# Kernel tuning notes

Measured on AMD Instinct MI355X. Metric: run time of the kernel, lower is better.

The kernel has to match this reference:

```python
import jax, jax.numpy as jnp
import numpy as np

# delta_rule mode: order=1, gate_type='k', linear=True, trick='derivative' (n=1 expansion is identity)
B, H, S, D = 1, 16, 4096, 64
CHUNK = 64  # max_chunk_size, divides S
EPS = 1e-6


def setup_inputs() -> dict:
    key = jax.random.key(0)
    kq, kk, kv, kb = jax.random.split(key, 4)
    return {
        "q": jax.random.normal(kq, (B, H, S, D), jnp.float32),
        "k": jax.random.normal(kk, (B, H, S, D), jnp.float32),
        "v": jax.random.normal(kv, (B, H, S, D), jnp.float32),
        "beta": jax.random.uniform(kb, (B, H, S), jnp.float32),
    }


def _ensure_stability(x, lo=-10000.0, hi=10000.0):
    c = (hi + lo) / 2
    x = jnp.clip(x, lo, hi)
    return jnp.nan_to_num(x, nan=c, posinf=hi, neginf=lo)


def _l2norm(x):
    return x / (jnp.linalg.norm(x, axis=-1, keepdims=True) + EPS)


def _forward(q, k, v, beta):
    Bq, Hq, Sq, Dq = q.shape
    C = CHUNK
    Nc = Sq // C
    q = _l2norm(q)
    k = _l2norm(k)
    # gate_type 'k': clamp(beta, 1e-6, 1-1e-6)
    g = jnp.clip(beta, EPS, 1.0 - EPS)[..., None]
    k_beta = k * g
    v_beta = v * g
    ch = lambda x: x.reshape(Bq, Hq, Nc, C, Dq)  # chunk_sequence
    qc, kc, kbc, vbc = map(ch, (q, k, k_beta, v_beta))

    # UT transform: attn = -(k_beta k^T) strictly lower; T = (I - attn)^{-1}
    # fast_invert_matrix (forward substitution) == unit-lower triangular solve
    attn = -jnp.einsum('bhnid,bhnjd->bhnij', kbc, kc)
    strict = jnp.tril(jnp.ones((C, C), bool), k=-1)
    attn = jnp.where(strict, attn, 0.0)
    eye = jnp.eye(C, dtype=q.dtype)
    Tm = jax.lax.linalg.triangular_solve(
        eye - attn, jnp.broadcast_to(eye, attn.shape),
        left_side=True, lower=True, unit_diagonal=True)
    W = jnp.einsum('bhnij,bhnjd->bhnid', Tm, kbc)
    U = jnp.einsum('bhnij,bhnjd->bhnid', Tm, vbc)

    # sequential_delta_product_scan, n_orders=1: per-token state == broadcast h0
    def step(h0, xs):
        q_c, w_c, u_c = xs  # each [B,H,C,D]; h0 [B,H,D,D]
        kth = jnp.einsum('bhcd,bhde->bhce', w_c, h0)      # w_s @ h_old per token
        u_val = u_c - kth
        o_inter = jnp.einsum('bhcd,bhde->bhce', q_c, h0)  # q_s @ h_old
        o_intra = q_c * u_val                              # elementwise, as in source
        # per-token Householder state update; only last token's state propagates (n_orders=1)
        h_new = h0 + w_c[:, :, -1, :, None] * u_val[:, :, -1, None, :]
        h_new = _ensure_stability(h_new)
        return h_new, o_intra + o_inter

    xs = (jnp.moveaxis(qc, 2, 0), jnp.moveaxis(W, 2, 0), jnp.moveaxis(U, 2, 0))
    h0 = jnp.zeros((Bq, Hq, Dq, Dq), q.dtype)
    _, outs = jax.lax.scan(step, h0, xs)  # [Nc, B, H, C, D]
    return jnp.moveaxis(outs, 0, 2).reshape(Bq, Hq, Sq, Dq)


def reference(q, k, v, beta):
    return _forward(q, k, v, beta)
```

## Files before the change

kernel.cpp:

```cpp
#include <hip/hip_runtime.h>
#include <math.h>

#define BHn 16
#define SLEN 4096
#define Dd 64
#define Cc 64
#define NCC 64
#define EPSF 1e-6f
#define PD 65

__global__ __launch_bounds__(256, 4) void kA(
    const float* __restrict__ kg, const float* __restrict__ vg,
    const float* __restrict__ betag, float* __restrict__ WTg, float* __restrict__ UTg,
    float* __restrict__ wlast, float* __restrict__ ulast)
{
    const int n = blockIdx.x, bh = blockIdx.y, tid = threadIdx.x;
    __shared__ float KT[64 * PD];
    __shared__ float SM[64 * PD];
    __shared__ float gl[64];

    const size_t base = ((size_t)bh * SLEN + (size_t)n * Cc) * Dd;

    if (tid < 64) {
        const float b = betag[(size_t)bh * SLEN + n * Cc + tid];
        gl[tid] = fminf(fmaxf(b, EPSF), 1.0f - EPSF);
    }
#pragma unroll
    for (int p = 0; p < 4; p++) {
        const int flat = p * 1024 + tid * 4;
        const int row = flat >> 6, d0 = flat & 63;
        const float4 a = *(const float4*)(kg + base + flat);
        float ss = a.x * a.x + a.y * a.y + a.z * a.z + a.w * a.w;
        ss += __shfl_xor(ss, 1); ss += __shfl_xor(ss, 2);
        ss += __shfl_xor(ss, 4); ss += __shfl_xor(ss, 8);
        const float inv = 1.0f / (sqrtf(ss) + EPSF);
        KT[(d0 + 0) * PD + row] = a.x * inv;
        KT[(d0 + 1) * PD + row] = a.y * inv;
        KT[(d0 + 2) * PD + row] = a.z * inv;
        KT[(d0 + 3) * PD + row] = a.w * inv;
    }
    __syncthreads();

    float sol[64];
    if (tid < 64) {
#pragma unroll
        for (int j4 = 0; j4 < 16; j4++) {
            const float4 t4 = *(const float4*)&KT[tid * PD + j4 * 4];
            sol[j4 * 4 + 0] = t4.x * gl[j4 * 4 + 0];
            sol[j4 * 4 + 1] = t4.y * gl[j4 * 4 + 1];
            sol[j4 * 4 + 2] = t4.z * gl[j4 * 4 + 2];
            sol[j4 * 4 + 3] = t4.w * gl[j4 * 4 + 3];
        }
    } else if (tid < 200) {
        const int t = tid - 64;
        int ti = (int)((sqrtf(8.0f * (float)t + 1.0f) - 1.0f) * 0.5f);
        while (ti * (ti + 1) / 2 > t) --ti;
        while ((ti + 1) * (ti + 2) / 2 <= t) ++ti;
        const int tj = t - ti * (ti + 1) / 2;
        const int i0 = ti * 4, j0 = tj * 4;
        float sa[4][4];
#pragma unroll
        for (int r = 0; r < 4; r++)
#pragma unroll
            for (int c2 = 0; c2 < 4; c2++) sa[r][c2] = 0.f;
        for (int d = 0; d < 64; d++) {
            const float4 a = *(const float4*)&KT[d * PD + i0];
            const float4 b = *(const float4*)&KT[d * PD + j0];
            const float av[4] = {a.x, a.y, a.z, a.w};
            const float bv[4] = {b.x, b.y, b.z, b.w};
#pragma unroll
            for (int r = 0; r < 4; r++)
#pragma unroll
                for (int c2 = 0; c2 < 4; c2++) sa[r][c2] += av[r] * bv[c2];
        }
#pragma unroll
        for (int r = 0; r < 4; r++) {
            const float gg = gl[i0 + r];
            *(float4*)&SM[(i0 + r) * PD + j0] =
                make_float4(sa[r][0] * gg, sa[r][1] * gg, sa[r][2] * gg, sa[r][3] * gg);
        }
    }
    __syncthreads();

#pragma unroll
    for (int p = 0; p < 4; p++) {
        const int flat = p * 1024 + tid * 4;
        const int row = flat >> 6, d0 = flat & 63;
        const float4 a = *(const float4*)(vg + base + flat);
        const float gg = gl[row];
        KT[(d0 + 0) * PD + row] = a.x * gg;
        KT[(d0 + 1) * PD + row] = a.y * gg;
        KT[(d0 + 2) * PD + row] = a.z * gg;
        KT[(d0 + 3) * PD + row] = a.w * gg;
    }
    __syncthreads();

    if (tid >= 64 && tid < 128) {
        const int c = tid - 64;
#pragma unroll
        for (int j4 = 0; j4 < 16; j4++) {
            const float4 t4 = *(const float4*)&KT[c * PD + j4 * 4];
            sol[j4 * 4 + 0] = t4.x; sol[j4 * 4 + 1] = t4.y;
            sol[j4 * 4 + 2] = t4.z; sol[j4 * 4 + 3] = t4.w;
        }
    }
    if (tid < 128) {
        const int c = tid & 63;
#pragma unroll
        for (int b = 0; b < 8; b++) {
            const int i0 = b * 8;
            float acc[8];
#pragma unroll
            for (int r = 0; r < 8; r++) acc[r] = sol[i0 + r];
#pragma unroll
            for (int j4 = 0; j4 < 2 * b; j4++) {
                const int j = j4 * 4;
                const float s0 = sol[j + 0], s1 = sol[j + 1];
                const float s2 = sol[j + 2], s3 = sol[j + 3];
#pragma unroll
                for (int r = 0; r < 8; r++) {
                    const float4 m4 = *(const float4*)&SM[(i0 + r) * PD + j];
                    acc[r] -= m4.x * s0 + m4.y * s1 + m4.z * s2 + m4.w * s3;
                }
            }
#pragma unroll
            for (int il = 1; il < 8; il++)
#pragma unroll
                for (int jl = 0; jl < il; jl++)
                    acc[il] -= SM[(i0 + il) * PD + i0 + jl] * acc[jl];
#pragma unroll
            for (int r = 0; r < 8; r++) sol[i0 + r] = acc[r];
        }
        float* dst = (tid < 64 ? WTg : UTg) +
                     (size_t)(bh * NCC + n) * Cc * Dd + (size_t)c * 64;
#pragma unroll
        for (int j4 = 0; j4 < 16; j4++)
            *(float4*)(dst + j4 * 4) = make_float4(sol[j4 * 4 + 0], sol[j4 * 4 + 1],
                                                   sol[j4 * 4 + 2], sol[j4 * 4 + 3]);
        float* lst = (tid < 64 ? wlast : ulast);
        lst[(size_t)(bh * NCC + n) * 64 + c] = sol[63];
    }
}

__global__ __launch_bounds__(256) void kB(
    const float* __restrict__ wlast, const float* __restrict__ ulast,
    float* __restrict__ Uvg)
{
    const int bh = blockIdx.x, tid = threadIdx.x;
    __shared__ float WL[64 * PD];
    __shared__ float UL[64 * PD];
    __shared__ float SM[64 * PD];
    const size_t gbase = (size_t)bh * NCC * 64;

#pragma unroll
    for (int p = 0; p < 4; p++) {
        const int flat = p * 1024 + tid * 4;
        const int m = flat >> 6, d = flat & 63;
        *(float4*)&WL[m * PD + d] = *(const float4*)(wlast + gbase + flat);
        *(float4*)&UL[m * PD + d] = *(const float4*)(ulast + gbase + flat);
    }
    __syncthreads();

    if (tid < 136) {
        int ti = (int)((sqrtf(8.0f * (float)tid + 1.0f) - 1.0f) * 0.5f);
        while (ti * (ti + 1) / 2 > tid) --ti;
        while ((ti + 1) * (ti + 2) / 2 <= tid) ++ti;
        const int tj = tid - ti * (ti + 1) / 2;
        const int i0 = ti * 4, j0 = tj * 4;
        float sa[4][4];
#pragma unroll
        for (int r = 0; r < 4; r++)
#pragma unroll
            for (int c2 = 0; c2 < 4; c2++) sa[r][c2] = 0.f;
        for (int d4 = 0; d4 < 16; d4++) {
            const int d = d4 * 4;
            float4 ar[4], bc[4];
#pragma unroll
            for (int r = 0; r < 4; r++) ar[r] = *(const float4*)&WL[(i0 + r) * PD + d];
#pragma unroll
            for (int c2 = 0; c2 < 4; c2++) bc[c2] = *(const float4*)&WL[(j0 + c2) * PD + d];
#pragma unroll
            for (int r = 0; r < 4; r++)
#pragma unroll
                for (int c2 = 0; c2 < 4; c2++)
                    sa[r][c2] += ar[r].x * bc[c2].x + ar[r].y * bc[c2].y +
                                 ar[r].z * bc[c2].z + ar[r].w * bc[c2].w;
        }
#pragma unroll
        for (int r = 0; r < 4; r++)
            *(float4*)&SM[(i0 + r) * PD + j0] =
                make_float4(sa[r][0], sa[r][1], sa[r][2], sa[r][3]);
    }
    __syncthreads();

    if (tid < 64) {
        const int e = tid;
        float sol[64];
#pragma unroll
        for (int m = 0; m < 64; m++) sol[m] = UL[m * PD + e];
#pragma unroll
        for (int b = 0; b < 8; b++) {
            const int i0 = b * 8;
            float acc[8];
#pragma unroll
            for (int r = 0; r < 8; r++) acc[r] = sol[i0 + r];
#pragma unroll
            for (int j4 = 0; j4 < 2 * b; j4++) {
                const int j = j4 * 4;
                const float s0 = sol[j + 0], s1 = sol[j + 1];
                const float s2 = sol[j + 2], s3 = sol[j + 3];
#pragma unroll
                for (int r = 0; r < 8; r++) {
                    const float4 m4 = *(const float4*)&SM[(i0 + r) * PD + j];
                    acc[r] -= m4.x * s0 + m4.y * s1 + m4.z * s2 + m4.w * s3;
                }
            }
#pragma unroll
            for (int il = 1; il < 8; il++)
#pragma unroll
                for (int jl = 0; jl < il; jl++)
                    acc[il] -= SM[(i0 + il) * PD + i0 + jl] * acc[jl];
#pragma unroll
            for (int r = 0; r < 8; r++) sol[i0 + r] = acc[r];
        }
#pragma unroll
        for (int m = 0; m < 64; m++) Uvg[gbase + (size_t)m * 64 + e] = sol[m];
    }
}

__global__ __launch_bounds__(256, 3) void kC(
    const float* __restrict__ qg, const float* __restrict__ WTg,
    const float* __restrict__ UTg, const float* __restrict__ wlast,
    const float* __restrict__ Uvg, float* __restrict__ outg)
{
    const int bx = blockIdx.x, bh = blockIdx.y, tid = threadIdx.x;
    __shared__ float X1[64 * 64];
    __shared__ float X2[64 * PD];
    __shared__ float HB[64 * 64];
    const size_t lbase = (size_t)bh * NCC * 64;
    const int t0 = (tid >> 4) * 4, e0 = (tid & 15) * 4;

    const int n = 63 - bx;
    const size_t qbase = ((size_t)bh * SLEN + (size_t)n * Cc) * Dd;
    const size_t wbase = (size_t)(bh * NCC + n) * Cc * Dd;

    float4 qa[4], wt[4];
    float qinv[4];
#pragma unroll
    for (int p = 0; p < 4; p++) {
        const int flat = p * 1024 + tid * 4;
        const int m = flat >> 6, d = flat & 63;
        *(float4*)&X1[m * 64 + d] = *(const float4*)(wlast + lbase + flat);
        *(float4*)&X2[m * PD + d] = *(const float4*)(Uvg + lbase + flat);
        qa[p] = *(const float4*)(qg + qbase + flat);
        float ss = qa[p].x * qa[p].x + qa[p].y * qa[p].y +
                   qa[p].z * qa[p].z + qa[p].w * qa[p].w;
        ss += __shfl_xor(ss, 1); ss += __shfl_xor(ss, 2);
        ss += __shfl_xor(ss, 4); ss += __shfl_xor(ss, 8);
        qinv[p] = 1.0f / (sqrtf(ss) + EPSF);
        wt[p] = *(const float4*)(WTg + wbase + flat);
    }
    __syncthreads();

    float ha[4][4];
#pragma unroll
    for (int r = 0; r < 4; r++)
#pragma unroll
        for (int c2 = 0; c2 < 4; c2++) ha[r][c2] = 0.f;
    for (int m = 0; m < n; m++) {
        const float4 a = *(const float4*)&X1[m * 64 + t0];
        const float4 b = *(const float4*)&X2[m * PD + e0];
        const float av[4] = {a.x, a.y, a.z, a.w};
        const float bv[4] = {b.x, b.y, b.z, b.w};
#pragma unroll
        for (int r = 0; r < 4; r++)
#pragma unroll
            for (int c2 = 0; c2 < 4; c2++) ha[r][c2] += av[r] * bv[c2];
    }
#pragma unroll
    for (int r = 0; r < 4; r++)
        *(float4*)&HB[(t0 + r) * 64 + e0] =
            make_float4(ha[r][0], ha[r][1], ha[r][2], ha[r][3]);
    __syncthreads();

#pragma unroll
    for (int p = 0; p < 4; p++) {
        const int flat = p * 1024 + tid * 4;
        const int d = flat >> 6, t = flat & 63;
        *(float4*)&X1[d * 64 + t] = wt[p];
        const int row = d, d0 = t;
        X2[(d0 + 0) * PD + row] = qa[p].x * qinv[p];
        X2[(d0 + 1) * PD + row] = qa[p].y * qinv[p];
        X2[(d0 + 2) * PD + row] = qa[p].z * qinv[p];
        X2[(d0 + 3) * PD + row] = qa[p].w * qinv[p];
    }
    __syncthreads();

    float kth[4][4], oin[4][4];
#pragma unroll
    for (int r = 0; r < 4; r++)
#pragma unroll
        for (int c2 = 0; c2 < 4; c2++) { kth[r][c2] = 0.f; oin[r][c2] = 0.f; }
#pragma unroll 4
    for (int d = 0; d < 64; d++) {
        const float4 wv = *(const float4*)&X1[d * 64 + t0];
        const float4 qv = *(const float4*)&X2[d * PD + t0];
        const float4 hv = *(const float4*)&HB[d * 64 + e0];
        const float wa[4] = {wv.x, wv.y, wv.z, wv.w};
        const float qa2[4] = {qv.x, qv.y, qv.z, qv.w};
        const float hv4[4] = {hv.x, hv.y, hv.z, hv.w};
#pragma unroll
        for (int r = 0; r < 4; r++)
#pragma unroll
            for (int c2 = 0; c2 < 4; c2++) {
                kth[r][c2] += wa[r] * hv4[c2];
                oin[r][c2] += qa2[r] * hv4[c2];
            }
    }

    float* oc = outg + qbase;
    float o4[4][4];
#pragma unroll
    for (int s = 0; s < 4; s++) {
        const float4 u4 = *(const float4*)(UTg + wbase + (size_t)(e0 + s) * 64 + t0);
        const float4 q4 = *(const float4*)&X2[(e0 + s) * PD + t0];
        o4[0][s] = q4.x * (u4.x - kth[0][s]) + oin[0][s];
        o4[1][s] = q4.y * (u4.y - kth[1][s]) + oin[1][s];
        o4[2][s] = q4.z * (u4.z - kth[2][s]) + oin[2][s];
        o4[3][s] = q4.w * (u4.w - kth[3][s]) + oin[3][s];
    }
#pragma unroll
    for (int r = 0; r < 4; r++)
        *(float4*)(oc + (size_t)(t0 + r) * 64 + e0) =
            make_float4(o4[r][0], o4[r][1], o4[r][2], o4[r][3]);
}

extern "C" void kernel_launch(void* const* d_in, const int* in_sizes, int n_in,
                              void* d_out, int out_size, void* d_ws, size_t ws_size,
                              hipStream_t stream) {
    const float* q    = (const float*)d_in[0];
    const float* k    = (const float*)d_in[1];
    const float* v    = (const float*)d_in[2];
    const float* beta = (const float*)d_in[3];
    float* out = (float*)d_out;

    float* WTg   = (float*)d_ws;
    float* UTg   = WTg + (size_t)BHn * NCC * Cc * Dd;
    float* wlast = UTg + (size_t)BHn * NCC * Cc * Dd;
    float* ulast = wlast + (size_t)BHn * NCC * 64;
    float* Uvg   = ulast + (size_t)BHn * NCC * 64;

    kA<<<dim3(NCC, BHn), 256, 0, stream>>>(k, v, beta, WTg, UTg, wlast, ulast);
    kB<<<dim3(BHn), 256, 0, stream>>>(wlast, ulast, Uvg);
    kC<<<dim3(64, BHn), 256, 0, stream>>>(q, WTg, UTg, wlast, Uvg, out);
}
```

Baseline: 84.30 us.

## Pack strict-lower triangle into per-lane registers and broadcast via readlane

Kernel kA now stores only the strictly lower triangle of the chunk's k_beta·k^T matrix, packed into a 2016-element padded shared array. Each lane loads 32 elements into registers, and the forward-substitution solve fetches matrix coefficients with readlane broadcasts instead of shared-memory reads. This is meant to cut LDS traffic and footprint in the serial triangular solve. In exchange it adds register pressure (32 extra floats per thread) and many scalar readlane instructions. The packing also assumes the 64 solving lanes of a wave each hold their own slice, and threads 64-127 sit in a second wavefront that reads lanes 0-63 of its own wave.

```diff
diff --git a/kernel.cpp b/kernel.cpp
--- a/kernel.cpp
+++ b/kernel.cpp
@@ -16,7 +16,7 @@
 {
     const int n = blockIdx.x, bh = blockIdx.y, tid = threadIdx.x;
     __shared__ float KT[64 * PD];
-    __shared__ float SM[64 * PD];
+    __shared__ float SMf[64 * 36];
     __shared__ float gl[64];
 
     const size_t base = ((size_t)bh * SLEN + (size_t)n * Cc) * Dd;
@@ -75,9 +75,16 @@
         }
 #pragma unroll
         for (int r = 0; r < 4; r++) {
-            const float gg = gl[i0 + r];
-            *(float4*)&SM[(i0 + r) * PD + j0] =
-                make_float4(sa[r][0] * gg, sa[r][1] * gg, sa[r][2] * gg, sa[r][3] * gg);
+            const int i = i0 + r;
+            const int eb = (i * (i - 1)) / 2 + j0;
+            const float gg = gl[i];
+#pragma unroll
+            for (int c2 = 0; c2 < 4; c2++) {
+                if (ti != tj || c2 < r) {
+                    const int e = eb + c2;
+                    SMf[36 * (e >> 5) + (e & 31)] = sa[r][c2] * gg;
+                }
+            }
         }
     }
     __syncthreads();
@@ -106,6 +113,16 @@
     }
     if (tid < 128) {
         const int c = tid & 63;
+        float sm[32];
+        {
+            const int lb = 36 * c;
+#pragma unroll
+            for (int r8 = 0; r8 < 8; r8++) {
+                const float4 t4 = *(const float4*)&SMf[lb + r8 * 4];
+                sm[r8 * 4 + 0] = t4.x; sm[r8 * 4 + 1] = t4.y;
+                sm[r8 * 4 + 2] = t4.z; sm[r8 * 4 + 3] = t4.w;
+            }
+        }
 #pragma unroll
         for (int b = 0; b < 8; b++) {
             const int i0 = b * 8;
@@ -113,21 +130,25 @@
 #pragma unroll
             for (int r = 0; r < 8; r++) acc[r] = sol[i0 + r];
 #pragma unroll
-            for (int j4 = 0; j4 < 2 * b; j4++) {
-                const int j = j4 * 4;
-                const float s0 = sol[j + 0], s1 = sol[j + 1];
-                const float s2 = sol[j + 2], s3 = sol[j + 3];
+            for (int j = 0; j < 8 * b; j++) {
+                const float sj = sol[j];
 #pragma unroll
                 for (int r = 0; r < 8; r++) {
-                    const float4 m4 = *(const float4*)&SM[(i0 + r) * PD + j];
-                    acc[r] -= m4.x * s0 + m4.y * s1 + m4.z * s2 + m4.w * s3;
+                    const int e = ((i0 + r) * (i0 + r - 1)) / 2 + j;
+                    const float s = __int_as_float(__builtin_amdgcn_readlane(
+                        __float_as_int(sm[e & 31]), e >> 5));
+                    acc[r] -= s * sj;
                 }
             }
 #pragma unroll
             for (int il = 1; il < 8; il++)
 #pragma unroll
-                for (int jl = 0; jl < il; jl++)
-                    acc[il] -= SM[(i0 + il) * PD + i0 + jl] * acc[jl];
+                for (int jl = 0; jl < il; jl++) {
+                    const int e = ((i0 + il) * (i0 + il - 1)) / 2 + i0 + jl;
+                    const float s = __int_as_float(__builtin_amdgcn_readlane(
+                        __float_as_int(sm[e & 31]), e >> 5));
+                    acc[il] -= s * acc[jl];
+                }
 #pragma unroll
             for (int r = 0; r < 8; r++) sol[i0 + r] = acc[r];
         }
```

New measurement: 92.42 us. +9.6%, slower.
